# Kernel optimization log

Measured on AMD Instinct MI355X. Metric: run time of the kernel, lower is better.

Reference implementation:

```python
import jax, jax.numpy as jnp
import numpy as np

B, M, N, T = 16, 16, 32, 80


def setup_inputs() -> dict:
    key = jax.random.key(0)
    ks = jax.random.split(key, 20)
    p = lambda k, shp: jax.random.normal(k, shp, jnp.float32) * 0.05
    return {
        "ego_traj": jax.random.normal(ks[0], (B, M, T, 6), jnp.float32),
        "ego_encoding": jax.random.normal(ks[1], (B, 256), jnp.float32),
        "agents_traj": jax.random.normal(ks[2], (B, M, N, T, 3), jnp.float32),
        "agents_states": jax.random.normal(ks[3], (B, N, 11), jnp.float32),
        # interaction_feature_encoder: Linear(10,64) -> ReLU -> Linear(64,256)
        "enc_w1": p(ks[4], (10, 64)), "enc_b1": p(ks[5], (64,)),
        "enc_w2": p(ks[6], (64, 256)), "enc_b2": p(ks[7], (256,)),
        # interaction_feature_decoder: Linear(256,64) -> ELU -> Linear(64,4) -> Sigmoid
        "dec_w1": p(ks[8], (256, 64)), "dec_b1": p(ks[9], (64,)),
        "dec_w2": p(ks[10], (64, 4)), "dec_b2": p(ks[11], (4,)),
        # weights_decoder: Linear(256,64) -> ELU -> Linear(64,8) -> Softplus
        "wd_w1": p(ks[12], (256, 64)), "wd_b1": p(ks[13], (64,)),
        "wd_w2": p(ks[14], (64, 8)), "wd_b2": p(ks[15], (8,)),
        "timesteps": 80,
    }


def reference(ego_traj, ego_encoding, agents_traj, agents_states,
              enc_w1, enc_b1, enc_w2, enc_b2,
              dec_w1, dec_b1, dec_w2, dec_b2,
              wd_w1, wd_b1, wd_w2, wd_b2, timesteps):
    Tm = timesteps
    # ---- hardcoded ego features: B,M,4 ----
    speed = ego_traj[:, :, :Tm, 3]
    acc = ego_traj[:, :, :Tm, 4]
    jerk = jnp.diff(acc, axis=-1) / 0.1
    jerk = jnp.concatenate([jerk[:, :, :1], jerk], axis=-1)
    curvature = ego_traj[:, :, :Tm, 5]
    lat_acc = speed ** 2 * curvature
    hard = jnp.stack([
        -jnp.clip(speed.mean(-1), 0.0, 15.0) / 15.0,
        jnp.clip(jnp.abs(acc).mean(-1), 0.0, 4.0) / 4.0,
        jnp.clip(jnp.abs(jerk).mean(-1), 0.0, 6.0) / 6.0,
        jnp.clip(jnp.abs(lat_acc).mean(-1), 0.0, 5.0) / 5.0,
    ], axis=-1)  # B,M,4

    # ---- latent interaction features (vectorized over M) ----
    agent_mask = (agents_states.sum(-1) != 0).astype(ego_traj.dtype)  # B,N
    ry = agents_traj[:, :, :, :Tm, 2] - ego_traj[:, :, None, :Tm, 2]  # B,M,N,T
    ry = jnp.arctan2(jnp.sin(ry), jnp.cos(ry))
    rp = agents_traj[:, :, :, :Tm, :2] - ego_traj[:, :, None, :Tm, :2]
    rp = jnp.stack([rp[..., 0] * jnp.cos(ry), rp[..., 1] * jnp.sin(ry)], axis=-1)
    av = jnp.diff(agents_traj[:, :, :, :Tm, :2], axis=-2) / 0.1
    av = jnp.concatenate([av[:, :, :, :1, :], av], axis=-2)
    evx = ego_traj[:, :, :Tm, 3] * jnp.cos(ego_traj[:, :, :Tm, 2])  # B,M,T
    evy = ego_traj[:, :, :Tm, 3] * jnp.sin(ego_traj[:, :, :Tm, 2])
    rv = jnp.stack([(av[..., 0] - evx[:, :, None]) * jnp.cos(ry),
                    (av[..., 1] - evy[:, :, None]) * jnp.sin(ry)], axis=-1)
    rel = jnp.concatenate([rp, ry[..., None], rv], axis=-1)  # B,M,N,T,5
    aattr = jnp.broadcast_to(agents_states[:, None, :, None, 6:], rel.shape[:4] + (5,))
    attr = jnp.concatenate([rel, aattr], axis=-1) * agent_mask[:, None, :, None, None]  # B,M,N,T,10
    h = jax.nn.relu(attr @ enc_w1 + enc_b1) @ enc_w2 + enc_b2  # B,M,N,T,256
    feat = h.max(axis=2).mean(axis=2)  # max over agents, mean over time -> B,M,256
    inter = jax.nn.sigmoid(jax.nn.elu(feat @ dec_w1 + dec_b1) @ dec_w2 + dec_b2)  # B,M,4

    # ---- weights (variable_cost=False -> ones_like encoding) ----
    enc_in = jnp.ones_like(ego_encoding)
    weights = jax.nn.softplus(jax.nn.elu(enc_in @ wd_w1 + wd_b1) @ wd_w2 + wd_b2)  # B,8

    # ---- collision cost: B,M ----
    dist = jnp.linalg.norm(ego_traj[:, :, None, :Tm, :2] - agents_traj[:, :, :, :Tm, :2], axis=-1)
    coll = (jnp.exp(-0.2 * dist ** 2) * agent_mask[:, None, :, None]).sum((-1, -2))

    feats = jnp.concatenate([hard, inter], axis=-1)  # B,M,8
    scores = -jnp.sum(feats * weights[:, None, :], axis=-1) - 10.0 * coll
    ego_mask = ego_traj.sum(-1).sum(-1) != 0  # B,M
    scores = jnp.where(ego_mask, scores, -jnp.inf)
    return scores, weights
```

## Files before the change

kernel.cpp:

```cpp
#include <hip/hip_runtime.h>
#include <hip/hip_fp16.h>
#include <math.h>
#include <string.h>

typedef __attribute__((ext_vector_type(8))) short short8;
typedef __attribute__((ext_vector_type(8))) _Float16 f16x8;
typedef __attribute__((ext_vector_type(4))) _Float16 h4;
typedef __attribute__((ext_vector_type(2))) _Float16 h2;
typedef __attribute__((ext_vector_type(4))) float f32x4;

#define NB 16
#define NM 16
#define NN 32
#define NT 80
#define TC 16
#define NP 5
#define CH 4
#define NCH 8

#define WS_WTS 0
#define WS_BF 16
#define WS_BB 8208
#define WS_BASE 24592
#define WS_BM_STRIDE 1344
#define WS_SC_OFF 1280

__device__ __forceinline__ short f2h(float f) {
  _Float16 h = (_Float16)f;
  short s; memcpy(&s, &h, 2); return s;
}
__device__ __forceinline__ unsigned h2bits(h2 h) {
  unsigned u; memcpy(&u, &h, 4); return u;
}
__device__ __forceinline__ h2 bits2h(unsigned u) {
  h2 h; memcpy(&h, &u, 4); return h;
}

__global__ void prep_kernel(const float* __restrict__ agents_states,
                            const float* __restrict__ enc_w1,
                            const float* __restrict__ enc_b1,
                            const float* __restrict__ enc_w2,
                            const float* __restrict__ wd_w1,
                            const float* __restrict__ wd_b1,
                            const float* __restrict__ wd_w2,
                            const float* __restrict__ wd_b2,
                            float* __restrict__ ws,
                            float* __restrict__ out) {
  const int blk = blockIdx.x;
  const int tid = threadIdx.x;
  if (blk < NB) {
    __shared__ float smask[NN];
    if (tid < NN) {
      const float* st = agents_states + ((size_t)blk * NN + tid) * 11;
      float s = 0.f;
      for (int i = 0; i < 11; ++i) s += st[i];
      smask[tid] = (s != 0.f) ? 1.f : 0.f;
    }
    __syncthreads();
    h2* bb = reinterpret_cast<h2*>(ws + WS_BB) + blk * (NN * 32);
    for (int e = tid; e < NN * 32; e += 256) {
      int n = e >> 5, jp = e & 31;
      const float* st = agents_states + ((size_t)blk * NN + n) * 11 + 6;
      float v[2];
#pragma unroll
      for (int hh = 0; hh < 2; ++hh) {
        int j = jp * 2 + hh;
        float acc = st[0] * enc_w1[5 * 64 + j] + st[1] * enc_w1[6 * 64 + j] +
                    st[2] * enc_w1[7 * 64 + j] + st[3] * enc_w1[8 * 64 + j] +
                    st[4] * enc_w1[9 * 64 + j];
        v[hh] = smask[n] * acc + enc_b1[j];
      }
      h2 r; r[0] = (_Float16)v[0]; r[1] = (_Float16)v[1];
      bb[e] = r;
    }
  } else if (blk < NB + 8) {
    const int g = tid >> 6;
    const int lane = tid & 63;
    const int s = (blk - NB) * 4 + g;
    const int wv = s >> 3, jb = (s >> 1) & 3, kt = s & 1;
    const int col = wv * 64 + jb * 16 + (lane & 15);
    const int krow = (lane >> 4) * 8;
    short8 v;
#pragma unroll
    for (int j = 0; j < 8; ++j)
      v[j] = f2h(enc_w2[(kt * 32 + krow + j) * 256 + col]);
    reinterpret_cast<short8*>(ws + WS_BF)[s * 64 + lane] = v;
  } else {
    __shared__ float s_part[4][64];
    __shared__ float sh[64];
    const int g = tid >> 6, j = tid & 63;
    {
      float a = 0.f;
#pragma unroll 8
      for (int i = 0; i < 64; ++i)
        a += wd_w1[(g * 64 + i) * 64 + j];
      s_part[g][j] = a;
    }
    __syncthreads();
    if (tid < 64) {
      float acc = wd_b1[tid] + ((s_part[0][tid] + s_part[1][tid]) +
                                (s_part[2][tid] + s_part[3][tid]));
      sh[tid] = acc > 0.f ? acc : expm1f(acc);
    }
    __syncthreads();
    if (tid < 8) {
      float acc = wd_b2[tid];
      for (int k = 0; k < 64; ++k) acc += sh[k] * wd_w2[k * 8 + tid];
      float sp = log1pf(__expf(acc));
      ws[WS_WTS + tid] = sp;
      for (int b = 0; b < NB; ++b) out[NB * NM + b * 8 + tid] = sp;
    }
  }
}

__global__ __launch_bounds__(256, 4) void score_partial(
    const float* __restrict__ ego_traj,
    const float* __restrict__ agents_traj,
    const float* __restrict__ agents_states,
    const float* __restrict__ enc_w1,
    float* __restrict__ ws)
{
  __shared__ h4 s_r01[NN][TC];
  __shared__ h4 s_r23[NN][TC];
  __shared__ h2 s_r4[NN][TC];
  __shared__ uint2 s_bb[NN][16];
  __shared__ __align__(16) char s_hid[2][CH][TC * 128];
  __shared__ float s_ego[TC][5];
  __shared__ float s_acc[TC + 2];
  __shared__ float s_spd[TC], s_lat[TC], s_egos[TC];
  __shared__ float s_mask[NN];
  __shared__ float s_cw[4];

  const int p = blockIdx.x;
  const int bm = blockIdx.y;
  const int t0 = p * TC;
  const int b = bm >> 4;
  const int tid = threadIdx.x;
  const int lane = tid & 63;
  const int wv = tid >> 6;

  float* ws_bm = ws + WS_BASE + (size_t)bm * WS_BM_STRIDE;

  if (tid < TC) {
    int i = tid;
    const float* e = ego_traj + ((size_t)bm * NT + (t0 + i)) * 6;
    float ex = e[0], ey = e[1], eh = e[2], spd = e[3], acc = e[4], cur = e[5];
    s_ego[i][0] = ex; s_ego[i][1] = ey; s_ego[i][2] = eh;
    s_ego[i][3] = spd * __cosf(eh);
    s_ego[i][4] = spd * __sinf(eh);
    s_spd[i] = spd;
    s_acc[i + 1] = acc;
    s_lat[i] = fabsf(spd * spd * cur);
    s_egos[i] = ex + ey + eh + spd + acc + cur;
  } else if (tid == TC) {
    int tp = (p == 0) ? 0 : (t0 - 1);
    s_acc[0] = ego_traj[((size_t)bm * NT + tp) * 6 + 4];
  } else if (tid >= 64 && tid < 64 + NN) {
    int n = tid - 64;
    const float* st = agents_states + ((size_t)b * NN + n) * 11;
    float s = 0.f;
    for (int i = 0; i < 11; ++i) s += st[i];
    s_mask[n] = (s != 0.f) ? 1.f : 0.f;
  }
  {
    const uint2* bbt = reinterpret_cast<const uint2*>(ws + WS_BB) + b * 512;
#pragma unroll
    for (int k = 0; k < 2; ++k) {
      int e = tid + k * 256;
      s_bb[e >> 4][e & 15] = bbt[e];
    }
  }

  const int jq = tid & 15;
  const int tt = tid >> 4;
  const int j0 = jq * 4;

  f16x8 Bf[4][2];
  {
    const f16x8* bft = reinterpret_cast<const f16x8*>(ws + WS_BF);
#pragma unroll
    for (int jb = 0; jb < 4; ++jb)
#pragma unroll
      for (int kt = 0; kt < 2; ++kt)
        Bf[jb][kt] = bft[((wv * 4 + jb) * 2 + kt) * 64 + lane];
  }

  h2 w1h[5][2];
#pragma unroll
  for (int f = 0; f < 5; ++f)
#pragma unroll
    for (int jp = 0; jp < 2; ++jp) {
      h2 r;
      r[0] = (_Float16)enc_w1[f * 64 + j0 + jp * 2];
      r[1] = (_Float16)enc_w1[f * 64 + j0 + jp * 2 + 1];
      w1h[f][jp] = r;
    }
  __syncthreads();

  {
    float collacc = 0.f;
    const float* atraj = agents_traj + (size_t)bm * (NN * NT * 3);
#pragma unroll
    for (int k = 0; k < 2; ++k) {
      int pp = tid + k * 256;
      int n = pp >> 4;
      int i = pp & 15;
      int tg = t0 + i;
      const float* bp = atraj + n * (NT * 3) + tg * 3;
      float ax = bp[0], ay = bp[1], ah = bp[2];
      float avx, avy;
      if (tg == 0) { avx = (bp[3] - ax) * 10.f; avy = (bp[4] - ay) * 10.f; }
      else         { avx = (ax - bp[-3]) * 10.f; avy = (ay - bp[-2]) * 10.f; }
      float ex = s_ego[i][0], ey = s_ego[i][1], eh = s_ego[i][2];
      float evx = s_ego[i][3], evy = s_ego[i][4];
      float m = s_mask[n];
      float ryr = ah - eh;
      float w = ryr - 6.283185307179586f * rintf(ryr * 0.15915494309189535f);
      float cy = __cosf(ryr), sy = __sinf(ryr);
      float dx = ax - ex, dy = ay - ey;
      float r0 = dx * cy * m, r1 = dy * sy * m, r2 = w * m;
      float r3 = (avx - evx) * cy * m, r4 = (avy - evy) * sy * m;
      h4 v01, v23; h2 v4;
      v01[0] = v01[1] = (_Float16)r0; v01[2] = v01[3] = (_Float16)r1;
      v23[0] = v23[1] = (_Float16)r2; v23[2] = v23[3] = (_Float16)r3;
      v4[0] = v4[1] = (_Float16)r4;
      s_r01[n][i] = v01;
      s_r23[n][i] = v23;
      s_r4[n][i] = v4;
      collacc += __expf(-0.2f * (dx * dx + dy * dy)) * m;
    }
#pragma unroll
    for (int off = 1; off < 64; off <<= 1) collacc += __shfl_xor(collacc, off);
    if (lane == 0) s_cw[wv] = collacc;
  }

  if (tid >= 251) {
    int which = tid - 251;
    float s = 0.f;
    if (which == 0)      { for (int i = 0; i < TC; ++i) s += s_spd[i]; }
    else if (which == 1) { for (int i = 0; i < TC; ++i) s += fabsf(s_acc[i + 1]); }
    else if (which == 2) {
      for (int i = 0; i < TC; ++i) {
        int ia = (p == 0 && i == 0) ? 2 : (i + 1);
        s += fabsf((s_acc[ia] - s_acc[ia - 1]) * 10.f);
      }
    }
    else if (which == 3) { for (int i = 0; i < TC; ++i) s += s_lat[i]; }
    else                 { for (int i = 0; i < TC; ++i) s += s_egos[i]; }
    ws_bm[WS_SC_OFF + p * 8 + which] = s;
  }

  const int tl = lane & 15, kg = lane >> 4;
  const int swr = (tl & 7) << 4;
  const int aoff0 = tl * 128 + ((kg * 16) ^ swr);
  const int aoff1 = tl * 128 + ((64 + kg * 16) ^ swr);
  const int wbyte = tt * 128 + ((jq * 8) ^ ((tt & 7) << 4));

  h2 z2; z2[0] = z2[1] = (_Float16)0.f;

  auto compute_chunk = [&](int c, int buf) {
#pragma unroll
    for (int nn = 0; nn < CH; ++nn) {
      const int n = c * CH + nn;
      h4 r01 = s_r01[n][tt];
      h4 r23 = s_r23[n][tt];
      h2 r4 = s_r4[n][tt];
      uint2 bb = s_bb[n][jq];
      h2 a0 = __builtin_shufflevector(r01, r01, 0, 1);
      h2 a1 = __builtin_shufflevector(r01, r01, 2, 3);
      h2 a2 = __builtin_shufflevector(r23, r23, 0, 1);
      h2 a3 = __builtin_shufflevector(r23, r23, 2, 3);
      uint2 u;
#pragma unroll
      for (int jp = 0; jp < 2; ++jp) {
        h2 ha = bits2h(jp ? bb.y : bb.x);
        ha = a0 * w1h[0][jp] + ha;
        ha = a1 * w1h[1][jp] + ha;
        ha = a2 * w1h[2][jp] + ha;
        ha = a3 * w1h[3][jp] + ha;
        ha = r4 * w1h[4][jp] + ha;
        ha = __builtin_elementwise_max(ha, z2);
        if (jp == 0) u.x = h2bits(ha); else u.y = h2bits(ha);
      }
      *reinterpret_cast<uint2*>(&s_hid[buf][nn][0] + wbyte) = u;
    }
  };

  f32x4 rmax[4];
#pragma unroll
  for (int jb = 0; jb < 4; ++jb)
    rmax[jb] = f32x4{-3e38f, -3e38f, -3e38f, -3e38f};

  auto mfma_step = [&](int buf) {
#pragma unroll
    for (int nn = 0; nn < CH; ++nn) {
      const char* slab = &s_hid[buf][nn][0];
      f16x8 A0 = *reinterpret_cast<const f16x8*>(slab + aoff0);
      f16x8 A1 = *reinterpret_cast<const f16x8*>(slab + aoff1);
#pragma unroll
      for (int jb = 0; jb < 4; ++jb) {
        f32x4 c = {0.f, 0.f, 0.f, 0.f};
        c = __builtin_amdgcn_mfma_f32_16x16x32_f16(A0, Bf[jb][0], c, 0, 0, 0);
        c = __builtin_amdgcn_mfma_f32_16x16x32_f16(A1, Bf[jb][1], c, 0, 0, 0);
        rmax[jb] = __builtin_elementwise_max(rmax[jb], c);
      }
    }
  };

  __syncthreads();
  compute_chunk(0, 0);
  __syncthreads();

  for (int c = 0; c < NCH; ++c) {
    if (c + 1 < NCH) compute_chunk(c + 1, (c + 1) & 1);
    mfma_step(c & 1);
    __syncthreads();
  }

  {
#pragma unroll
    for (int jb = 0; jb < 4; ++jb) {
      float s = (rmax[jb][0] + rmax[jb][1]) + (rmax[jb][2] + rmax[jb][3]);
      s += __shfl_xor(s, 16);
      s += __shfl_xor(s, 32);
      if (lane < 16)
        ws_bm[p * 256 + wv * 64 + jb * 16 + lane] = s;
    }
  }
  if (tid == 0)
    ws_bm[WS_SC_OFF + p * 8 + 5] = s_cw[0] + s_cw[1] + s_cw[2] + s_cw[3];
}

__global__ void combine_kernel(const float* __restrict__ ws,
                               const float* __restrict__ enc_b2,
                               const float* __restrict__ dec_w1,
                               const float* __restrict__ dec_b1,
                               const float* __restrict__ dec_w2,
                               const float* __restrict__ dec_b2,
                               float* __restrict__ out_scores) {
  __shared__ float s_feat[256];
  __shared__ float s_dhp[4][64];
  __shared__ float s_dh[64];
  __shared__ float s_hard[4];
  __shared__ float s_inter[4];
  __shared__ float s_mc[2];
  const int bm = blockIdx.x;
  const int tid = threadIdx.x;
  const float* wb = ws + WS_BASE + (size_t)bm * WS_BM_STRIDE;

  {
    int c = tid;
    float f = 0.f;
#pragma unroll
    for (int pp = 0; pp < NP; ++pp) f += wb[pp * 256 + c];
    s_feat[c] = f * (1.f / NT) + enc_b2[c];
  }
  const float* sc = wb + WS_SC_OFF;
  if (tid < 6) {
    float s = 0.f;
#pragma unroll
    for (int pp = 0; pp < NP; ++pp) s += sc[pp * 8 + tid];
    if (tid == 0) s_hard[0] = -fminf(fmaxf(s * (1.f / NT), 0.f), 15.f) * (1.f / 15.f);
    if (tid == 1) s_hard[1] = fminf(fmaxf(s * (1.f / NT), 0.f), 4.f) * 0.25f;
    if (tid == 2) s_hard[2] = fminf(fmaxf(s * (1.f / NT), 0.f), 6.f) * (1.f / 6.f);
    if (tid == 3) s_hard[3] = fminf(fmaxf(s * (1.f / NT), 0.f), 5.f) * 0.2f;
    if (tid == 4) s_mc[0] = s;
    if (tid == 5) s_mc[1] = s;
  }
  __syncthreads();

  {
    const int q = tid >> 6, j = tid & 63;
    float a = 0.f;
#pragma unroll 8
    for (int i = 0; i < 64; ++i)
      a += s_feat[q * 64 + i] * dec_w1[(q * 64 + i) * 64 + j];
    s_dhp[q][j] = a;
  }
  __syncthreads();
  if (tid < 64) {
    float acc = dec_b1[tid] + ((s_dhp[0][tid] + s_dhp[1][tid]) +
                               (s_dhp[2][tid] + s_dhp[3][tid]));
    s_dh[tid] = acc > 0.f ? acc : expm1f(acc);
  }
  __syncthreads();

  if (tid < 4) {
    float acc = dec_b2[tid];
    for (int k = 0; k < 64; ++k) acc += s_dh[k] * dec_w2[k * 4 + tid];
    s_inter[tid] = 1.f / (1.f + __expf(-acc));
  }
  __syncthreads();

  if (tid == 0) {
    const float* wts = ws + WS_WTS;
    float scv = 0.f;
#pragma unroll
    for (int i = 0; i < 4; ++i) scv += s_hard[i] * wts[i];
#pragma unroll
    for (int i = 0; i < 4; ++i) scv += s_inter[i] * wts[4 + i];
    scv = -scv - 10.f * s_mc[1];
    if (s_mc[0] == 0.f) scv = -INFINITY;
    out_scores[bm] = scv;
  }
}

extern "C" void kernel_launch(void* const* d_in, const int* in_sizes, int n_in,
                              void* d_out, int out_size, void* d_ws, size_t ws_size,
                              hipStream_t stream) {
  const float* ego_traj      = (const float*)d_in[0];
  const float* agents_traj   = (const float*)d_in[2];
  const float* agents_states = (const float*)d_in[3];
  const float* enc_w1 = (const float*)d_in[4];
  const float* enc_b1 = (const float*)d_in[5];
  const float* enc_w2 = (const float*)d_in[6];
  const float* enc_b2 = (const float*)d_in[7];
  const float* dec_w1 = (const float*)d_in[8];
  const float* dec_b1 = (const float*)d_in[9];
  const float* dec_w2 = (const float*)d_in[10];
  const float* dec_b2 = (const float*)d_in[11];
  const float* wd_w1 = (const float*)d_in[12];
  const float* wd_b1 = (const float*)d_in[13];
  const float* wd_w2 = (const float*)d_in[14];
  const float* wd_b2 = (const float*)d_in[15];

  float* out = (float*)d_out;
  float* ws = (float*)d_ws;

  prep_kernel<<<NB + 9, 256, 0, stream>>>(agents_states, enc_w1, enc_b1, enc_w2,
                                          wd_w1, wd_b1, wd_w2, wd_b2, ws, out);
  dim3 grid(NP, NB * NM);
  score_partial<<<grid, 256, 0, stream>>>(
      ego_traj, agents_traj, agents_states, enc_w1, ws);
  combine_kernel<<<NB * NM, 256, 0, stream>>>(
      ws, enc_b2, dec_w1, dec_b1, dec_w2, dec_b2, out);
}
```

Baseline: 41.12 us.

## Widen time chunk to 20 steps, cutting blocks per trajectory from five to four

Each block now covers 20 timesteps instead of 16, so each (b,m) pair needs 4 blocks instead of 5 and per-block fixed costs are paid less often. The 4 extra rows per chunk go through a second MFMA tile; only 4 of its 16 rows are distinct and only lanes holding those rows contribute to the reduction. The thread-to-(column, row) mapping is swapped and the trajectory loop gains a third guarded iteration. In exchange, MFMA work per chunk doubles for a quarter more useful rows, and shared arrays must be sized for 20 rows.

```diff
diff --git a/kernel.cpp b/kernel.cpp
--- a/kernel.cpp
+++ b/kernel.cpp
@@ -13,8 +13,8 @@
 #define NM 16
 #define NN 32
 #define NT 80
-#define TC 16
-#define NP 5
+#define TC 20
+#define NP 4
 #define CH 4
 #define NCH 8
 
@@ -22,8 +22,8 @@
 #define WS_BF 16
 #define WS_BB 8208
 #define WS_BASE 24592
-#define WS_BM_STRIDE 1344
-#define WS_SC_OFF 1280
+#define WS_BM_STRIDE 1088
+#define WS_SC_OFF 1024
 
 __device__ __forceinline__ short f2h(float f) {
   _Float16 h = (_Float16)f;
@@ -171,9 +171,10 @@
     }
   }
 
-  const int jq = tid & 15;
-  const int tt = tid >> 4;
-  const int j0 = jq * 4;
+  const int jq = tid >> 4;
+  const int tt = tid & 15;
+  const int j0 = (jq & 3) * 4 + wv * 0;
+  const int j0g = jq * 4;
 
   f16x8 Bf[4][2];
   {
@@ -191,8 +192,8 @@
 #pragma unroll
     for (int jp = 0; jp < 2; ++jp) {
       h2 r;
-      r[0] = (_Float16)enc_w1[f * 64 + j0 + jp * 2];
-      r[1] = (_Float16)enc_w1[f * 64 + j0 + jp * 2 + 1];
+      r[0] = (_Float16)enc_w1[f * 64 + j0g + jp * 2];
+      r[1] = (_Float16)enc_w1[f * 64 + j0g + jp * 2 + 1];
       w1h[f][jp] = r;
     }
   __syncthreads();
@@ -201,33 +202,35 @@
     float collacc = 0.f;
     const float* atraj = agents_traj + (size_t)bm * (NN * NT * 3);
 #pragma unroll
-    for (int k = 0; k < 2; ++k) {
+    for (int k = 0; k < 3; ++k) {
       int pp = tid + k * 256;
-      int n = pp >> 4;
-      int i = pp & 15;
-      int tg = t0 + i;
-      const float* bp = atraj + n * (NT * 3) + tg * 3;
-      float ax = bp[0], ay = bp[1], ah = bp[2];
-      float avx, avy;
-      if (tg == 0) { avx = (bp[3] - ax) * 10.f; avy = (bp[4] - ay) * 10.f; }
-      else         { avx = (ax - bp[-3]) * 10.f; avy = (ay - bp[-2]) * 10.f; }
-      float ex = s_ego[i][0], ey = s_ego[i][1], eh = s_ego[i][2];
-      float evx = s_ego[i][3], evy = s_ego[i][4];
-      float m = s_mask[n];
-      float ryr = ah - eh;
-      float w = ryr - 6.283185307179586f * rintf(ryr * 0.15915494309189535f);
-      float cy = __cosf(ryr), sy = __sinf(ryr);
-      float dx = ax - ex, dy = ay - ey;
-      float r0 = dx * cy * m, r1 = dy * sy * m, r2 = w * m;
-      float r3 = (avx - evx) * cy * m, r4 = (avy - evy) * sy * m;
-      h4 v01, v23; h2 v4;
-      v01[0] = v01[1] = (_Float16)r0; v01[2] = v01[3] = (_Float16)r1;
-      v23[0] = v23[1] = (_Float16)r2; v23[2] = v23[3] = (_Float16)r3;
-      v4[0] = v4[1] = (_Float16)r4;
-      s_r01[n][i] = v01;
-      s_r23[n][i] = v23;
-      s_r4[n][i] = v4;
-      collacc += __expf(-0.2f * (dx * dx + dy * dy)) * m;
+      if (pp < NN * TC) {
+        int n = pp / TC;
+        int i = pp - n * TC;
+        int tg = t0 + i;
+        const float* bp = atraj + n * (NT * 3) + tg * 3;
+        float ax = bp[0], ay = bp[1], ah = bp[2];
+        float avx, avy;
+        if (tg == 0) { avx = (bp[3] - ax) * 10.f; avy = (bp[4] - ay) * 10.f; }
+        else         { avx = (ax - bp[-3]) * 10.f; avy = (ay - bp[-2]) * 10.f; }
+        float ex = s_ego[i][0], ey = s_ego[i][1], eh = s_ego[i][2];
+        float evx = s_ego[i][3], evy = s_ego[i][4];
+        float m = s_mask[n];
+        float ryr = ah - eh;
+        float w = ryr - 6.283185307179586f * rintf(ryr * 0.15915494309189535f);
+        float cy = __cosf(ryr), sy = __sinf(ryr);
+        float dx = ax - ex, dy = ay - ey;
+        float r0 = dx * cy * m, r1 = dy * sy * m, r2 = w * m;
+        float r3 = (avx - evx) * cy * m, r4 = (avy - evy) * sy * m;
+        h4 v01, v23; h2 v4;
+        v01[0] = v01[1] = (_Float16)r0; v01[2] = v01[3] = (_Float16)r1;
+        v23[0] = v23[1] = (_Float16)r2; v23[2] = v23[3] = (_Float16)r3;
+        v4[0] = v4[1] = (_Float16)r4;
+        s_r01[n][i] = v01;
+        s_r23[n][i] = v23;
+        s_r4[n][i] = v4;
+        collacc += __expf(-0.2f * (dx * dx + dy * dy)) * m;
+      }
     }
 #pragma unroll
     for (int off = 1; off < 64; off <<= 1) collacc += __shfl_xor(collacc, off);
@@ -254,42 +257,58 @@
   const int swr = (tl & 7) << 4;
   const int aoff0 = tl * 128 + ((kg * 16) ^ swr);
   const int aoff1 = tl * 128 + ((64 + kg * 16) ^ swr);
-  const int wbyte = tt * 128 + ((jq * 8) ^ ((tt & 7) << 4));
+  const int tl4 = tl & 3;
+  const int swr2 = tl4 << 4;
+  const int aoff2_0 = (16 + tl4) * 128 + ((kg * 16) ^ swr2);
+  const int aoff2_1 = (16 + tl4) * 128 + ((64 + kg * 16) ^ swr2);
+  const int wbyte  = tt * 128 + ((jq * 8 & 127) ^ ((tt & 7) << 4));
+  const int wbyte2 = (16 + tt) * 128 + ((jq * 8 & 127) ^ ((tt & 7) << 4));
 
   h2 z2; z2[0] = z2[1] = (_Float16)0.f;
+
+  auto gemm1_row = [&](int n, int i, uint2 bb) -> uint2 {
+    h4 r01 = s_r01[n][i];
+    h4 r23 = s_r23[n][i];
+    h2 r4 = s_r4[n][i];
+    h2 a0 = __builtin_shufflevector(r01, r01, 0, 1);
+    h2 a1 = __builtin_shufflevector(r01, r01, 2, 3);
+    h2 a2 = __builtin_shufflevector(r23, r23, 0, 1);
+    h2 a3 = __builtin_shufflevector(r23, r23, 2, 3);
+    uint2 u;
+#pragma unroll
+    for (int jp = 0; jp < 2; ++jp) {
+      h2 ha = bits2h(jp ? bb.y : bb.x);
+      ha = a0 * w1h[0][jp] + ha;
+      ha = a1 * w1h[1][jp] + ha;
+      ha = a2 * w1h[2][jp] + ha;
+      ha = a3 * w1h[3][jp] + ha;
+      ha = r4 * w1h[4][jp] + ha;
+      ha = __builtin_elementwise_max(ha, z2);
+      if (jp == 0) u.x = h2bits(ha); else u.y = h2bits(ha);
+    }
+    return u;
+  };
 
   auto compute_chunk = [&](int c, int buf) {
 #pragma unroll
     for (int nn = 0; nn < CH; ++nn) {
       const int n = c * CH + nn;
-      h4 r01 = s_r01[n][tt];
-      h4 r23 = s_r23[n][tt];
-      h2 r4 = s_r4[n][tt];
       uint2 bb = s_bb[n][jq];
-      h2 a0 = __builtin_shufflevector(r01, r01, 0, 1);
-      h2 a1 = __builtin_shufflevector(r01, r01, 2, 3);
-      h2 a2 = __builtin_shufflevector(r23, r23, 0, 1);
-      h2 a3 = __builtin_shufflevector(r23, r23, 2, 3);
-      uint2 u;
-#pragma unroll
-      for (int jp = 0; jp < 2; ++jp) {
-        h2 ha = bits2h(jp ? bb.y : bb.x);
-        ha = a0 * w1h[0][jp] + ha;
-        ha = a1 * w1h[1][jp] + ha;
-        ha = a2 * w1h[2][jp] + ha;
-        ha = a3 * w1h[3][jp] + ha;
-        ha = r4 * w1h[4][jp] + ha;
-        ha = __builtin_elementwise_max(ha, z2);
-        if (jp == 0) u.x = h2bits(ha); else u.y = h2bits(ha);
+      uint2 u = gemm1_row(n, tt, bb);
+      *reinterpret_cast<uint2*>(&s_hid[buf][nn][0] + wbyte) = u;
+      if (tt < 4) {
+        uint2 u2 = gemm1_row(n, 16 + tt, bb);
+        *reinterpret_cast<uint2*>(&s_hid[buf][nn][0] + wbyte2) = u2;
       }
-      *reinterpret_cast<uint2*>(&s_hid[buf][nn][0] + wbyte) = u;
     }
   };
 
-  f32x4 rmax[4];
-#pragma unroll
-  for (int jb = 0; jb < 4; ++jb)
+  f32x4 rmax[4], rmax2[4];
+#pragma unroll
+  for (int jb = 0; jb < 4; ++jb) {
     rmax[jb] = f32x4{-3e38f, -3e38f, -3e38f, -3e38f};
+    rmax2[jb] = f32x4{-3e38f, -3e38f, -3e38f, -3e38f};
+  }
 
   auto mfma_step = [&](int buf) {
 #pragma unroll
@@ -297,12 +316,18 @@
       const char* slab = &s_hid[buf][nn][0];
       f16x8 A0 = *reinterpret_cast<const f16x8*>(slab + aoff0);
       f16x8 A1 = *reinterpret_cast<const f16x8*>(slab + aoff1);
+      f16x8 A20 = *reinterpret_cast<const f16x8*>(slab + aoff2_0);
+      f16x8 A21 = *reinterpret_cast<const f16x8*>(slab + aoff2_1);
 #pragma unroll
       for (int jb = 0; jb < 4; ++jb) {
         f32x4 c = {0.f, 0.f, 0.f, 0.f};
         c = __builtin_amdgcn_mfma_f32_16x16x32_f16(A0, Bf[jb][0], c, 0, 0, 0);
         c = __builtin_amdgcn_mfma_f32_16x16x32_f16(A1, Bf[jb][1], c, 0, 0, 0);
         rmax[jb] = __builtin_elementwise_max(rmax[jb], c);
+        f32x4 c2 = {0.f, 0.f, 0.f, 0.f};
+        c2 = __builtin_amdgcn_mfma_f32_16x16x32_f16(A20, Bf[jb][0], c2, 0, 0, 0);
+        c2 = __builtin_amdgcn_mfma_f32_16x16x32_f16(A21, Bf[jb][1], c2, 0, 0, 0);
+        rmax2[jb] = __builtin_elementwise_max(rmax2[jb], c2);
       }
     }
   };
@@ -321,6 +346,8 @@
 #pragma unroll
     for (int jb = 0; jb < 4; ++jb) {
       float s = (rmax[jb][0] + rmax[jb][1]) + (rmax[jb][2] + rmax[jb][3]);
+      if (kg == 0)
+        s += (rmax2[jb][0] + rmax2[jb][1]) + (rmax2[jb][2] + rmax2[jb][3]);
       s += __shfl_xor(s, 16);
       s += __shfl_xor(s, 32);
       if (lane < 16)
```

New measurement: 74.52 us. 81.2% more time.
